# Performance work log

Measured on AMD Instinct MI355X. Metric: run time of the kernel, lower is better.

## Reference

```python
import jax, jax.numpy as jnp
import numpy as np

D_MODEL = 1024
N_HEADS = 16
D_HEAD = D_MODEL // N_HEADS
B, T = 4, 2048


def setup_inputs() -> dict:
    key = jax.random.key(0)
    ks = jax.random.split(key, 9)
    s = 0.02
    return {
        "x": jax.random.normal(ks[0], (B, T, D_MODEL), dtype=jnp.float32),
        "Wq": jax.random.normal(ks[1], (D_MODEL, D_MODEL), dtype=jnp.float32) * s,
        "bq": jnp.zeros((D_MODEL,), dtype=jnp.float32),
        "Wk": jax.random.normal(ks[2], (D_MODEL, D_MODEL), dtype=jnp.float32) * s,
        "bk": jnp.zeros((D_MODEL,), dtype=jnp.float32),
        "Wv": jax.random.normal(ks[3], (D_MODEL, D_MODEL), dtype=jnp.float32) * s,
        "bv": jnp.zeros((D_MODEL,), dtype=jnp.float32),
        "Wo": jax.random.normal(ks[4], (D_MODEL, D_MODEL), dtype=jnp.float32) * s,
        "bo": jnp.zeros((D_MODEL,), dtype=jnp.float32),
    }


def reference(x, Wq, bq, Wk, bk, Wv, bv, Wo, bo):
    # Dropout in eval mode (identity), as standard for a correctness baseline.
    Bx, Tx, _ = x.shape
    # torch nn.Linear: y = x @ W.T + b
    Q = x @ Wq.T + bq
    K = x @ Wk.T + bk
    V = x @ Wv.T + bv
    # [B, T, H, Dh] -> [B, H, T, Dh]
    Q = Q.reshape(Bx, Tx, N_HEADS, D_HEAD).transpose(0, 2, 1, 3)
    K = K.reshape(Bx, Tx, N_HEADS, D_HEAD).transpose(0, 2, 1, 3)
    V = V.reshape(Bx, Tx, N_HEADS, D_HEAD).transpose(0, 2, 1, 3)
    scale = 1.0 / jnp.sqrt(jnp.float32(D_HEAD))
    scores = jnp.einsum("bhqd,bhkd->bhqk", Q, K) * scale  # [B,H,T,T]
    # additive causal mask: -1e6 above the diagonal (matches torch.triu trick)
    mask = jnp.triu(jnp.full((Tx, Tx), -1000000.0, dtype=scores.dtype), k=1)
    scores = scores + mask
    attn = jax.nn.softmax(scores, axis=-1)
    out = jnp.einsum("bhqk,bhkd->bhqd", attn, V)  # [B,H,T,Dh]
    out = out.transpose(0, 2, 1, 3).reshape(Bx, Tx, D_MODEL)
    out = out @ Wo.T + bo
    return out
```

## Files before the change

### kernel.cpp

```cpp
#include <hip/hip_runtime.h>
#include <stdint.h>

#define DM 1024
#define HEADS 16
#define DH 64
#define BQ 4
#define TT 2048
#define MTOT (BQ*TT)
#define NQT (TT/64)

typedef __attribute__((ext_vector_type(8))) __bf16 bf16x8;
typedef __attribute__((ext_vector_type(4))) float f32x4;
typedef __attribute__((ext_vector_type(4))) uint32_t u32x4;
typedef unsigned short u16;
typedef __attribute__((ext_vector_type(8))) unsigned short u16x8;

__device__ __forceinline__ u16 f2b(float f) {
  uint32_t u = __builtin_bit_cast(uint32_t, f);
  u = (u + 0x7fffu + ((u >> 16) & 1u)) >> 16;
  return (u16)u;
}

__device__ __forceinline__ uint32_t cvtpk(float lo, float hi) {
  uint32_t r;
  asm("v_cvt_pk_bf16_f32 %0, %1, %2" : "=v"(r) : "v"(lo), "v"(hi));
  return r;
}

__device__ __forceinline__ void gload_lds16(const u16* g, u16* l) {
  __builtin_amdgcn_global_load_lds(
      (const __attribute__((address_space(1))) void*)g,
      (__attribute__((address_space(3))) void*)l, 16, 0, 0);
}

#define NX (MTOT * DM / 4)
#define NW (DM * DM / 4)
__global__ __launch_bounds__(256) void cast_all(const float* __restrict__ x,
                                                const float* __restrict__ Wq,
                                                const float* __restrict__ Wk,
                                                const float* __restrict__ Wv,
                                                const float* __restrict__ Wo,
                                                u16* __restrict__ xb,
                                                u16* __restrict__ wqkvb,
                                                u16* __restrict__ wob) {
  int i = blockIdx.x * 256 + threadIdx.x;
  const float* src; u16* dst;
  if (i < NX)               { src = x;  dst = xb; }
  else if (i < NX + NW)     { src = Wq; dst = wqkvb;          i -= NX; }
  else if (i < NX + 2 * NW) { src = Wk; dst = wqkvb + 4 * NW; i -= NX + NW; }
  else if (i < NX + 3 * NW) { src = Wv; dst = wqkvb + 8 * NW; i -= NX + 2 * NW; }
  else                      { src = Wo; dst = wob;            i -= NX + 3 * NW; }
  float4 v = ((const float4*)src)[i];
  ushort4 o;
  o.x = f2b(v.x); o.y = f2b(v.y); o.z = f2b(v.z); o.w = f2b(v.w);
  ((ushort4*)dst)[i] = o;
}

#define BKq 32
#define NKq (DM / BKq)
#define SLOT_A (256 * BKq)
#define SLOT_E (2 * SLOT_A)

__global__ __launch_bounds__(512, 2) void gemm_qkv8(const u16* __restrict__ A,
                                                    const u16* __restrict__ W,
                                                    const float* __restrict__ bq,
                                                    const float* __restrict__ bk,
                                                    const float* __restrict__ bv,
                                                    u16* __restrict__ Qo,
                                                    u16* __restrict__ Ko,
                                                    u16* __restrict__ Vto,
                                                    float qs) {
  __shared__ u16 lds[4 * SLOT_E];
  const int tid = threadIdx.x, lane = tid & 63, wave = tid >> 6;
  const int fr = lane & 15, g = lane >> 4;
  const int wm = wave >> 2, wn = wave & 3;

  int bid = blockIdx.x;
  bid = (bid & 7) * 48 + (bid >> 3);
  const int bx = bid % 12, by = bid / 12;
  const int m0 = by * 256, n0 = bx * 256;

  const int srow = tid >> 2;
  const int schunk = (tid & 3) ^ ((tid >> 3) & 3);
  const u16* gA0 = A + (size_t)(m0 + srow) * DM + schunk * 8;
  const u16* gA1 = gA0 + (size_t)128 * DM;
  const u16* gB0 = W + (size_t)(n0 + srow) * DM + schunk * 8;
  const u16* gB1 = gB0 + (size_t)128 * DM;
  const int dA0 = wave * 512;
  const int dA1 = 4096 + wave * 512;
  const int dB0 = SLOT_A + wave * 512;
  const int dB1 = SLOT_A + 4096 + wave * 512;

#define STAGEQ(slot, kt) {                                   \
    u16* ls = &lds[(slot) * SLOT_E];                         \
    const int ke = (kt) * BKq;                               \
    gload_lds16(gA0 + ke, ls + dA0);                         \
    gload_lds16(gA1 + ke, ls + dA1);                         \
    gload_lds16(gB0 + ke, ls + dB0);                         \
    gload_lds16(gB1 + ke, ls + dB1); }

  const int rchunk = (g ^ ((fr >> 1) & 3)) * 8;
  const int offA = (wm * 128 + fr) * 32 + rchunk;
  const int offB = SLOT_A + (wn * 64 + fr) * 32 + rchunk;

  f32x4 acc[8][4];
#pragma unroll
  for (int mi = 0; mi < 8; ++mi)
#pragma unroll
    for (int ni = 0; ni < 4; ++ni) acc[mi][ni] = (f32x4){0.f, 0.f, 0.f, 0.f};

  bf16x8 afA[8], bfA[4], afB[8], bfB[4];

#define READQ(AFv, BFv, kt) {                                \
    const u16* sl = &lds[((kt) & 3) * SLOT_E];               \
    _Pragma("unroll")                                        \
    for (int mi = 0; mi < 8; ++mi)                           \
      AFv[mi] = *(const bf16x8*)&sl[offA + mi * 512];        \
    _Pragma("unroll")                                        \
    for (int ni = 0; ni < 4; ++ni)                           \
      BFv[ni] = *(const bf16x8*)&sl[offB + ni * 512]; }

#define MFMAQ(AFv, BFv) {                                    \
    __builtin_amdgcn_s_setprio(1);                           \
    _Pragma("unroll")                                        \
    for (int mi = 0; mi < 8; ++mi)                           \
      _Pragma("unroll")                                      \
      for (int ni = 0; ni < 4; ++ni)                         \
        acc[mi][ni] = __builtin_amdgcn_mfma_f32_16x16x32_bf16(AFv[mi], BFv[ni], acc[mi][ni], 0, 0, 0); \
    __builtin_amdgcn_s_setprio(0); }

#define WAIT4 asm volatile("s_waitcnt vmcnt(4)" ::: "memory"); \
              asm volatile("s_barrier" ::: "memory");
#define WAIT0 asm volatile("s_waitcnt vmcnt(0)" ::: "memory"); \
              asm volatile("s_barrier" ::: "memory");

  STAGEQ(0, 0)
  STAGEQ(1, 1)
  STAGEQ(2, 2)
  asm volatile("s_waitcnt vmcnt(8)" ::: "memory");
  asm volatile("s_barrier" ::: "memory");
  READQ(afA, bfA, 0)

  for (int kt = 0; kt < NKq - 4; kt += 2) {
    WAIT4
    READQ(afB, bfB, kt + 1)
    MFMAQ(afA, bfA)
    STAGEQ((kt + 3) & 3, kt + 3)
    WAIT4
    READQ(afA, bfA, kt + 2)
    MFMAQ(afB, bfB)
    STAGEQ((kt + 4) & 3, kt + 4)
  }
  WAIT4
  READQ(afB, bfB, NKq - 3)
  MFMAQ(afA, bfA)
  STAGEQ((NKq - 1) & 3, NKq - 1)
  WAIT4
  READQ(afA, bfA, NKq - 2)
  MFMAQ(afB, bfB)
  WAIT0
  READQ(afB, bfB, NKq - 1)
  MFMAQ(afA, bfA)
  MFMAQ(afB, bfB)

  const int g4 = g * 4;
  const int seg = n0 >> 10;
  const int nbase = (n0 & 1023) + wn * 64 + fr;
  if (seg == 0) {
#pragma unroll
    for (int ni = 0; ni < 4; ++ni) {
      const int cgl = nbase + ni * 16;
      const float bb = bq[cgl];
      const int hh = cgl >> 6, d = cgl & 63;
#pragma unroll
      for (int mi = 0; mi < 8; ++mi) {
        const int m = m0 + wm * 128 + mi * 16 + g4;
        const int bi = m >> 11, t = m & 2047;
        u16* dst = &Qo[(((size_t)bi * HEADS + hh) * TT + t) * DH + d];
#pragma unroll
        for (int j = 0; j < 4; ++j)
          dst[(size_t)j * DH] = f2b((acc[mi][ni][j] + bb) * qs);
      }
    }
  } else if (seg == 1) {
#pragma unroll
    for (int ni = 0; ni < 4; ++ni) {
      const int cgl = nbase + ni * 16;
      const float bb = bk[cgl];
      const int hh = cgl >> 6, d = cgl & 63;
#pragma unroll
      for (int mi = 0; mi < 8; ++mi) {
        const int m = m0 + wm * 128 + mi * 16 + g4;
        const int bi = m >> 11, t = m & 2047;
        u16* dst = &Ko[(((size_t)bi * HEADS + hh) * TT + t) * DH + d];
#pragma unroll
        for (int j = 0; j < 4; ++j)
          dst[(size_t)j * DH] = f2b(acc[mi][ni][j] + bb);
      }
    }
  } else {
#pragma unroll
    for (int ni = 0; ni < 4; ++ni) {
      const int cgl = nbase + ni * 16;
      const float bb = bv[cgl];
      const int hh = cgl >> 6, d = cgl & 63;
#pragma unroll
      for (int mi = 0; mi < 8; ++mi) {
        const int t0 = (m0 + wm * 128 + mi * 16 + g4) & 2047;
        const int bi = (m0 + wm * 128 + mi * 16 + g4) >> 11;
        const int w64 = t0 & 63;
        const int pos = (t0 & ~63) | (((w64 >> 5) & 1) << 5) | (((w64 >> 2) & 3) << 3) |
                        (((w64 >> 4) & 1) << 2);
        ushort4 o;
        o.x = f2b(acc[mi][ni][0] + bb);
        o.y = f2b(acc[mi][ni][1] + bb);
        o.z = f2b(acc[mi][ni][2] + bb);
        o.w = f2b(acc[mi][ni][3] + bb);
        *(ushort4*)&Vto[(((size_t)bi * HEADS + hh) * DH + d) * TT + pos] = o;
      }
    }
  }
#undef STAGEQ
#undef READQ
#undef MFMAQ
#undef WAIT4
#undef WAIT0
}

__global__ __launch_bounds__(256) void gemm_out(const u16* __restrict__ A,
                                                const u16* __restrict__ Bw,
                                                const float* __restrict__ bias,
                                                float* __restrict__ outp) {
  __shared__ u16 As[128 * 32];
  __shared__ u16 Bs[128 * 32];
  const int tid = threadIdx.x;
  const int lane = tid & 63, wave = tid >> 6;
  const int wr = wave >> 1, wc = wave & 1;
  const int m0 = blockIdx.y * 128, n0 = blockIdx.x * 128;

  f32x4 acc[4][4];
#pragma unroll
  for (int m = 0; m < 4; ++m)
#pragma unroll
    for (int n = 0; n < 4; ++n) acc[m][n] = (f32x4){0.f, 0.f, 0.f, 0.f};

  const int srow = wave * 32 + (lane >> 2);
  const int scol = (lane & 3) * 8;
  const u16* gA = A + (size_t)(m0 + srow) * DM + scol;
  const u16* gB = Bw + (size_t)(n0 + srow) * DM + scol;
  u16* lA = &As[wave * 32 * 32];
  u16* lB = &Bs[wave * 32 * 32];
  const int fr = lane & 15;
  const int k8 = (lane >> 4) * 8;

  for (int k0 = 0; k0 < DM; k0 += 32) {
    __syncthreads();
    gload_lds16(gA + k0, lA);
    gload_lds16(gA + k0 + 16 * DM, lA + 16 * 32);
    gload_lds16(gB + k0, lB);
    gload_lds16(gB + k0 + 16 * DM, lB + 16 * 32);
    __syncthreads();
    bf16x8 af[4], bfr[4];
#pragma unroll
    for (int m = 0; m < 4; ++m)
      af[m] = *(const bf16x8*)&As[(wr * 64 + m * 16 + fr) * 32 + k8];
#pragma unroll
    for (int n = 0; n < 4; ++n)
      bfr[n] = *(const bf16x8*)&Bs[(wc * 64 + n * 16 + fr) * 32 + k8];
#pragma unroll
    for (int m = 0; m < 4; ++m)
#pragma unroll
      for (int n = 0; n < 4; ++n)
        acc[m][n] = __builtin_amdgcn_mfma_f32_16x16x32_bf16(af[m], bfr[n], acc[m][n], 0, 0, 0);
  }

#pragma unroll
  for (int m = 0; m < 4; ++m) {
    const int rg = m0 + wr * 64 + m * 16 + (lane >> 4) * 4;
#pragma unroll
    for (int n = 0; n < 4; ++n) {
      const int cg = n0 + wc * 64 + n * 16 + fr;
      const float bb = bias[cg];
#pragma unroll
      for (int j = 0; j < 4; ++j)
        outp[(size_t)(rg + j) * DM + cg] = acc[m][n][j] + bb;
    }
  }
}

__global__ __launch_bounds__(256) void attn_fwd(const u16* __restrict__ Q,
                                                const u16* __restrict__ K,
                                                const u16* __restrict__ Vt,
                                                u16* __restrict__ O) {
  const int o_ = blockIdx.x;
  const int r_ = o_ & 7, q_ = o_ >> 3;
  const int gidx = r_ * 8 + (q_ >> 4);
  const int pj = q_ & 15;
  const int b = gidx >> 4, h = gidx & 15;
  const int tid = threadIdx.x, lane = tid & 63, wave = tid >> 6;
  __shared__ u16 Ks[64 * 64];
  __shared__ u16 Vs[64 * 64];

  const size_t bh = ((size_t)b * HEADS + h) * TT;
  const size_t vbse = ((size_t)b * HEADS + h) * DH;
  const int fr = lane & 15, g = lane >> 4;
  const int sr = tid >> 2;
  const int sc0 = tid & 3;

  const int sw1 = (sc0 ^ (sr & 7)) * 8;
  const int sw2 = ((sc0 + 4) ^ (sr & 7)) * 8;
  const int sgc = sc0 * 8;
  const int rk0 = (g ^ (fr & 7)) * 8;
  const int rk1 = ((4 + g) ^ (fr & 7)) * 8;

  for (int pass = 0; pass < 2; ++pass) {
    const int qt = pass ? pj : (NQT - 1 - pj);
    const int q0 = qt * 64;
    const int qrow = q0 + wave * 16 + fr;
    const int k8 = g * 8;
    const bf16x8 qf0 = *(const bf16x8*)&Q[(bh + qrow) * DH + k8];
    const bf16x8 qf1 = *(const bf16x8*)&Q[(bh + qrow) * DH + 32 + k8];

    float lsum = 0.f;
    f32x4 oacc[4];
#pragma unroll
    for (int c = 0; c < 4; ++c) oacc[c] = (f32x4){0.f, 0.f, 0.f, 0.f};

    for (int kvb = 0; kvb <= qt; ++kvb) {
      const int kv0 = kvb * 64;
      {
        const u16* kg = &K[(bh + kv0 + sr) * DH + sgc];
        u16x8 ka = *(const u16x8*)kg;
        u16x8 kc = *(const u16x8*)(kg + 32);
        const u16* vg = &Vt[(vbse + sr) * TT + kv0 + sgc];
        u16x8 va = *(const u16x8*)vg;
        u16x8 vc = *(const u16x8*)(vg + 32);
        *(u16x8*)&Ks[sr * 64 + sw1] = ka;
        *(u16x8*)&Ks[sr * 64 + sw2] = kc;
        *(u16x8*)&Vs[sr * 64 + sw1] = va;
        *(u16x8*)&Vs[sr * 64 + sw2] = vc;
      }
      __syncthreads();

      f32x4 s[4];
      __builtin_amdgcn_s_setprio(1);
#pragma unroll
      for (int c = 0; c < 4; ++c) {
        bf16x8 kb0 = *(const bf16x8*)&Ks[(c * 16 + fr) * 64 + rk0];
        bf16x8 kb1 = *(const bf16x8*)&Ks[(c * 16 + fr) * 64 + rk1];
        f32x4 t = (f32x4){0.f, 0.f, 0.f, 0.f};
        t = __builtin_amdgcn_mfma_f32_16x16x32_bf16(kb0, qf0, t, 0, 0, 0);
        t = __builtin_amdgcn_mfma_f32_16x16x32_bf16(kb1, qf1, t, 0, 0, 0);
        s[c] = t;
      }
      __builtin_amdgcn_s_setprio(0);

      if (kvb == qt) {
#pragma unroll
        for (int c = 0; c < 4; ++c) {
          const int colg = kv0 + c * 16 + 4 * g;
#pragma unroll
          for (int r = 0; r < 4; ++r)
            if (colg + r > qrow) s[c][r] = -1e30f;
        }
      }

      float rs = 0.f;
      uint32_t pk[8];
#pragma unroll
      for (int c = 0; c < 4; ++c) {
        float p0 = __builtin_amdgcn_exp2f(s[c][0]);
        float p1 = __builtin_amdgcn_exp2f(s[c][1]);
        float p2 = __builtin_amdgcn_exp2f(s[c][2]);
        float p3 = __builtin_amdgcn_exp2f(s[c][3]);
        rs += (p0 + p1) + (p2 + p3);
        pk[2 * c] = cvtpk(p0, p1);
        pk[2 * c + 1] = cvtpk(p2, p3);
      }
      rs += __shfl_xor(rs, 16);
      rs += __shfl_xor(rs, 32);
      lsum += rs;

      const bf16x8 pa0 = __builtin_bit_cast(bf16x8, (u32x4){pk[0], pk[1], pk[2], pk[3]});
      const bf16x8 pa1 = __builtin_bit_cast(bf16x8, (u32x4){pk[4], pk[5], pk[6], pk[7]});

      __builtin_amdgcn_s_setprio(1);
#pragma unroll
      for (int c = 0; c < 4; ++c) {
        bf16x8 vb0 = *(const bf16x8*)&Vs[(c * 16 + fr) * 64 + rk0];
        bf16x8 vb1 = *(const bf16x8*)&Vs[(c * 16 + fr) * 64 + rk1];
        oacc[c] = __builtin_amdgcn_mfma_f32_16x16x32_bf16(vb0, pa0, oacc[c], 0, 0, 0);
        oacc[c] = __builtin_amdgcn_mfma_f32_16x16x32_bf16(vb1, pa1, oacc[c], 0, 0, 0);
      }
      __builtin_amdgcn_s_setprio(0);
      __syncthreads();
    }

    const float inv = 1.f / lsum;
#pragma unroll
    for (int c = 0; c < 4; ++c) {
      ushort4 o;
      o.x = f2b(oacc[c][0] * inv);
      o.y = f2b(oacc[c][1] * inv);
      o.z = f2b(oacc[c][2] * inv);
      o.w = f2b(oacc[c][3] * inv);
      *(ushort4*)&O[((size_t)b * TT + qrow) * DM + h * DH + c * 16 + 4 * g] = o;
    }
  }
}

extern "C" void kernel_launch(void* const* d_in, const int* in_sizes, int n_in,
                              void* d_out, int out_size, void* d_ws, size_t ws_size,
                              hipStream_t stream) {
  const float* x  = (const float*)d_in[0];
  const float* Wq = (const float*)d_in[1];
  const float* bq = (const float*)d_in[2];
  const float* Wk = (const float*)d_in[3];
  const float* bk = (const float*)d_in[4];
  const float* Wv = (const float*)d_in[5];
  const float* bv = (const float*)d_in[6];
  const float* Wo = (const float*)d_in[7];
  const float* bo = (const float*)d_in[8];

  char* w = (char*)d_ws;
  u16* xb    = (u16*)w; w += (size_t)MTOT * DM * 2;
  u16* Wqkvb = (u16*)w; w += (size_t)3 * DM * DM * 2;
  u16* Wob   = (u16*)w; w += (size_t)DM * DM * 2;
  u16* Qb    = (u16*)w; w += (size_t)MTOT * DM * 2;
  u16* Kb    = (u16*)w; w += (size_t)MTOT * DM * 2;
  u16* Vtb   = (u16*)w; w += (size_t)MTOT * DM * 2;
  u16* AOb   = (u16*)w; w += (size_t)MTOT * DM * 2;

  cast_all<<<(NX + 4 * NW) / 256, 256, 0, stream>>>(x, Wq, Wk, Wv, Wo, xb, Wqkvb, Wob);

  const float qs = 0.125f * 1.44269504f;
  gemm_qkv8<<<384, 512, 0, stream>>>(xb, Wqkvb, bq, bk, bv, Qb, Kb, Vtb, qs);

  attn_fwd<<<1024, 256, 0, stream>>>(Qb, Kb, Vtb, AOb);

  gemm_out<<<dim3(DM / 128, MTOT / 128), 256, 0, stream>>>(AOb, Wob, bo, (float*)d_out);
}
```

Measured before the change: 166.3 us.

## Pipeline output projection GEMM with multi-stage LDS and split QKV stage loop

Replaces the simple single-buffered output-projection GEMM with a 512-thread, 256x128-tile kernel that uses a 4-slot direct-to-LDS prefetch pipeline with swizzled reads and counted vmcnt waits. It also splits each QKV GEMM k-step into two halves, with an extra barrier so the A and B tile loads are issued between MFMA halves. The aim is to hide global-load latency and remove per-step full syncs. The trade-offs are more LDS per block, which may limit occupancy, and extra barriers in the QKV loop.

```diff
diff --git a/kernel.cpp b/kernel.cpp
--- a/kernel.cpp
+++ b/kernel.cpp
@@ -91,11 +91,14 @@
   const int dB0 = SLOT_A + wave * 512;
   const int dB1 = SLOT_A + 4096 + wave * 512;
 
-#define STAGEQ(slot, kt) {                                   \
+#define STAGE_Ah(slot, kt) {                                 \
     u16* ls = &lds[(slot) * SLOT_E];                         \
     const int ke = (kt) * BKq;                               \
     gload_lds16(gA0 + ke, ls + dA0);                         \
-    gload_lds16(gA1 + ke, ls + dA1);                         \
+    gload_lds16(gA1 + ke, ls + dA1); }
+#define STAGE_Bh(slot, kt) {                                 \
+    u16* ls = &lds[(slot) * SLOT_E];                         \
+    const int ke = (kt) * BKq;                               \
     gload_lds16(gB0 + ke, ls + dB0);                         \
     gload_lds16(gB1 + ke, ls + dB1); }
 
@@ -111,57 +114,73 @@
 
   bf16x8 afA[8], bfA[4], afB[8], bfB[4];
 
-#define READQ(AFv, BFv, kt) {                                \
+#define READ_P1(AFv, BFv, kt) {                              \
     const u16* sl = &lds[((kt) & 3) * SLOT_E];               \
     _Pragma("unroll")                                        \
-    for (int mi = 0; mi < 8; ++mi)                           \
+    for (int mi = 0; mi < 4; ++mi)                           \
       AFv[mi] = *(const bf16x8*)&sl[offA + mi * 512];        \
     _Pragma("unroll")                                        \
     for (int ni = 0; ni < 4; ++ni)                           \
       BFv[ni] = *(const bf16x8*)&sl[offB + ni * 512]; }
-
-#define MFMAQ(AFv, BFv) {                                    \
+#define READ_P2(AFv, kt) {                                   \
+    const u16* sl = &lds[((kt) & 3) * SLOT_E];               \
+    _Pragma("unroll")                                        \
+    for (int mi = 4; mi < 8; ++mi)                           \
+      AFv[mi] = *(const bf16x8*)&sl[offA + mi * 512]; }
+
+#define MFMA_P1(AFv, BFv) {                                  \
     __builtin_amdgcn_s_setprio(1);                           \
     _Pragma("unroll")                                        \
-    for (int mi = 0; mi < 8; ++mi)                           \
+    for (int mi = 0; mi < 4; ++mi)                           \
       _Pragma("unroll")                                      \
       for (int ni = 0; ni < 4; ++ni)                         \
         acc[mi][ni] = __builtin_amdgcn_mfma_f32_16x16x32_bf16(AFv[mi], BFv[ni], acc[mi][ni], 0, 0, 0); \
     __builtin_amdgcn_s_setprio(0); }
-
-#define WAIT4 asm volatile("s_waitcnt vmcnt(4)" ::: "memory"); \
-              asm volatile("s_barrier" ::: "memory");
-#define WAIT0 asm volatile("s_waitcnt vmcnt(0)" ::: "memory"); \
-              asm volatile("s_barrier" ::: "memory");
-
-  STAGEQ(0, 0)
-  STAGEQ(1, 1)
-  STAGEQ(2, 2)
+#define MFMA_P2(AFv, BFv) {                                  \
+    __builtin_amdgcn_s_setprio(1);                           \
+    _Pragma("unroll")                                        \
+    for (int mi = 4; mi < 8; ++mi)                           \
+      _Pragma("unroll")                                      \
+      for (int ni = 0; ni < 4; ++ni)                         \
+        acc[mi][ni] = __builtin_amdgcn_mfma_f32_16x16x32_bf16(AFv[mi], BFv[ni], acc[mi][ni], 0, 0, 0); \
+    __builtin_amdgcn_s_setprio(0); }
+
+#define BARQ asm volatile("s_barrier" ::: "memory");
+#define WAIT4 asm volatile("s_waitcnt vmcnt(4)" ::: "memory"); BARQ
+#define WAIT0 asm volatile("s_waitcnt vmcnt(0)" ::: "memory"); BARQ
+
+#define STEP(AFc, BFc, AFn, BFn, kt, DO_STAGE) {             \
+    WAIT4                                                    \
+    READ_P1(AFn, BFn, (kt) + 1)                              \
+    MFMA_P1(AFc, BFc)                                        \
+    if (DO_STAGE) STAGE_Ah(((kt) + 3) & 3, (kt) + 3)         \
+    BARQ                                                     \
+    READ_P2(AFn, (kt) + 1)                                   \
+    MFMA_P2(AFc, BFc)                                        \
+    if (DO_STAGE) STAGE_Bh(((kt) + 3) & 3, (kt) + 3) }
+
+  STAGE_Ah(0, 0) STAGE_Bh(0, 0)
+  STAGE_Ah(1, 1) STAGE_Bh(1, 1)
+  STAGE_Ah(2, 2) STAGE_Bh(2, 2)
   asm volatile("s_waitcnt vmcnt(8)" ::: "memory");
   asm volatile("s_barrier" ::: "memory");
-  READQ(afA, bfA, 0)
+  READ_P1(afA, bfA, 0)
+  READ_P2(afA, 0)
 
   for (int kt = 0; kt < NKq - 4; kt += 2) {
-    WAIT4
-    READQ(afB, bfB, kt + 1)
-    MFMAQ(afA, bfA)
-    STAGEQ((kt + 3) & 3, kt + 3)
-    WAIT4
-    READQ(afA, bfA, kt + 2)
-    MFMAQ(afB, bfB)
-    STAGEQ((kt + 4) & 3, kt + 4)
+    STEP(afA, bfA, afB, bfB, kt, true)
+    STEP(afB, bfB, afA, bfA, kt + 1, true)
   }
-  WAIT4
-  READQ(afB, bfB, NKq - 3)
-  MFMAQ(afA, bfA)
-  STAGEQ((NKq - 1) & 3, NKq - 1)
-  WAIT4
-  READQ(afA, bfA, NKq - 2)
-  MFMAQ(afB, bfB)
+  STEP(afA, bfA, afB, bfB, NKq - 4, true)
+  STEP(afB, bfB, afA, bfA, NKq - 3, false)
   WAIT0
-  READQ(afB, bfB, NKq - 1)
-  MFMAQ(afA, bfA)
-  MFMAQ(afB, bfB)
+  READ_P1(afB, bfB, NKq - 1)
+  MFMA_P1(afA, bfA)
+  BARQ
+  READ_P2(afB, NKq - 1)
+  MFMA_P2(afA, bfA)
+  MFMA_P1(afB, bfB)
+  MFMA_P2(afB, bfB)
 
   const int g4 = g * 4;
   const int seg = n0 >> 10;
@@ -220,72 +239,132 @@
       }
     }
   }
-#undef STAGEQ
-#undef READQ
-#undef MFMAQ
+#undef STAGE_Ah
+#undef STAGE_Bh
+#undef READ_P1
+#undef READ_P2
+#undef MFMA_P1
+#undef MFMA_P2
+#undef STEP
+#undef BARQ
 #undef WAIT4
 #undef WAIT0
 }
 
-__global__ __launch_bounds__(256) void gemm_out(const u16* __restrict__ A,
-                                                const u16* __restrict__ Bw,
-                                                const float* __restrict__ bias,
-                                                float* __restrict__ outp) {
-  __shared__ u16 As[128 * 32];
-  __shared__ u16 Bs[128 * 32];
-  const int tid = threadIdx.x;
-  const int lane = tid & 63, wave = tid >> 6;
-  const int wr = wave >> 1, wc = wave & 1;
-  const int m0 = blockIdx.y * 128, n0 = blockIdx.x * 128;
+#define SLOT_OA (256 * 32)
+#define SLOT_OB (128 * 32)
+#define SLOT_OE (SLOT_OA + SLOT_OB)
+
+__global__ __launch_bounds__(512, 2) void gemm_out8(const u16* __restrict__ A,
+                                                    const u16* __restrict__ Bw,
+                                                    const float* __restrict__ bias,
+                                                    float* __restrict__ outp) {
+  __shared__ u16 lds[4 * SLOT_OE];
+  const int tid = threadIdx.x, lane = tid & 63, wave = tid >> 6;
+  const int fr = lane & 15, g = lane >> 4;
+  const int wm = wave >> 1, wn = wave & 1;
+
+  const int bx = blockIdx.x >> 5, by = blockIdx.x & 31;
+  const int m0 = by * 256, n0 = bx * 128;
+
+  const int srow = tid >> 2;
+  const int schunk = (tid & 3) ^ ((tid >> 3) & 3);
+  const u16* gA0 = A + (size_t)(m0 + srow) * DM + schunk * 8;
+  const u16* gA1 = gA0 + (size_t)128 * DM;
+  const u16* gB0 = Bw + (size_t)(n0 + srow) * DM + schunk * 8;
+  const int dA0 = wave * 512;
+  const int dA1 = 4096 + wave * 512;
+  const int dB0 = SLOT_OA + wave * 512;
+
+#define STAGEO(slot, kt) {                                   \
+    u16* ls = &lds[(slot) * SLOT_OE];                        \
+    const int ke = (kt) * 32;                                \
+    gload_lds16(gA0 + ke, ls + dA0);                         \
+    gload_lds16(gA1 + ke, ls + dA1);                         \
+    gload_lds16(gB0 + ke, ls + dB0); }
+
+  const int rchunk = (g ^ ((fr >> 1) & 3)) * 8;
+  const int offA = (wm * 64 + fr) * 32 + rchunk;
+  const int offB = SLOT_OA + (wn * 64 + fr) * 32 + rchunk;
 
   f32x4 acc[4][4];
 #pragma unroll
-  for (int m = 0; m < 4; ++m)
-#pragma unroll
-    for (int n = 0; n < 4; ++n) acc[m][n] = (f32x4){0.f, 0.f, 0.f, 0.f};
-
-  const int srow = wave * 32 + (lane >> 2);
-  const int scol = (lane & 3) * 8;
-  const u16* gA = A + (size_t)(m0 + srow) * DM + scol;
-  const u16* gB = Bw + (size_t)(n0 + srow) * DM + scol;
-  u16* lA = &As[wave * 32 * 32];
-  u16* lB = &Bs[wave * 32 * 32];
-  const int fr = lane & 15;
-  const int k8 = (lane >> 4) * 8;
-
-  for (int k0 = 0; k0 < DM; k0 += 32) {
-    __syncthreads();
-    gload_lds16(gA + k0, lA);
-    gload_lds16(gA + k0 + 16 * DM, lA + 16 * 32);
-    gload_lds16(gB + k0, lB);
-    gload_lds16(gB + k0 + 16 * DM, lB + 16 * 32);
-    __syncthreads();
-    bf16x8 af[4], bfr[4];
-#pragma unroll
-    for (int m = 0; m < 4; ++m)
-      af[m] = *(const bf16x8*)&As[(wr * 64 + m * 16 + fr) * 32 + k8];
-#pragma unroll
-    for (int n = 0; n < 4; ++n)
-      bfr[n] = *(const bf16x8*)&Bs[(wc * 64 + n * 16 + fr) * 32 + k8];
-#pragma unroll
-    for (int m = 0; m < 4; ++m)
-#pragma unroll
-      for (int n = 0; n < 4; ++n)
-        acc[m][n] = __builtin_amdgcn_mfma_f32_16x16x32_bf16(af[m], bfr[n], acc[m][n], 0, 0, 0);
+  for (int mi = 0; mi < 4; ++mi)
+#pragma unroll
+    for (int ni = 0; ni < 4; ++ni) acc[mi][ni] = (f32x4){0.f, 0.f, 0.f, 0.f};
+
+  bf16x8 afA[4], bfA[4], afB[4], bfB[4];
+
+#define READO(AFv, BFv, kt) {                                \
+    const u16* sl = &lds[((kt) & 3) * SLOT_OE];              \
+    _Pragma("unroll")                                        \
+    for (int mi = 0; mi < 4; ++mi)                           \
+      AFv[mi] = *(const bf16x8*)&sl[offA + mi * 512];        \
+    _Pragma("unroll")                                        \
+    for (int ni = 0; ni < 4; ++ni)                           \
+      BFv[ni] = *(const bf16x8*)&sl[offB + ni * 512]; }
+
+#define MFMAO(AFv, BFv) {                                    \
+    __builtin_amdgcn_s_setprio(1);                           \
+    _Pragma("unroll")                                        \
+    for (int mi = 0; mi < 4; ++mi)                           \
+      _Pragma("unroll")                                      \
+      for (int ni = 0; ni < 4; ++ni)                         \
+        acc[mi][ni] = __builtin_amdgcn_mfma_f32_16x16x32_bf16(AFv[mi], BFv[ni], acc[mi][ni], 0, 0, 0); \
+    __builtin_amdgcn_s_setprio(0); }
+
+#define OW3 asm volatile("s_waitcnt vmcnt(3)" ::: "memory"); \
+            asm volatile("s_barrier" ::: "memory");
+#define OW0 asm volatile("s_waitcnt vmcnt(0)" ::: "memory"); \
+            asm volatile("s_barrier" ::: "memory");
+
+  STAGEO(0, 0)
+  STAGEO(1, 1)
+  STAGEO(2, 2)
+  asm volatile("s_waitcnt vmcnt(6)" ::: "memory");
+  asm volatile("s_barrier" ::: "memory");
+  READO(afA, bfA, 0)
+
+  for (int kt = 0; kt < 28; kt += 2) {
+    OW3
+    READO(afB, bfB, kt + 1)
+    MFMAO(afA, bfA)
+    STAGEO((kt + 3) & 3, kt + 3)
+    OW3
+    READO(afA, bfA, kt + 2)
+    MFMAO(afB, bfB)
+    STAGEO((kt + 4) & 3, kt + 4)
   }
-
-#pragma unroll
-  for (int m = 0; m < 4; ++m) {
-    const int rg = m0 + wr * 64 + m * 16 + (lane >> 4) * 4;
-#pragma unroll
-    for (int n = 0; n < 4; ++n) {
-      const int cg = n0 + wc * 64 + n * 16 + fr;
+  OW3
+  READO(afB, bfB, 29)
+  MFMAO(afA, bfA)
+  STAGEO(3, 31)
+  OW3
+  READO(afA, bfA, 30)
+  MFMAO(afB, bfB)
+  OW0
+  READO(afB, bfB, 31)
+  MFMAO(afA, bfA)
+  MFMAO(afB, bfB)
+
+  const int g4 = g * 4;
+#pragma unroll
+  for (int mi = 0; mi < 4; ++mi) {
+    const int rg = m0 + wm * 64 + mi * 16 + g4;
+#pragma unroll
+    for (int ni = 0; ni < 4; ++ni) {
+      const int cg = n0 + wn * 64 + ni * 16 + fr;
       const float bb = bias[cg];
 #pragma unroll
       for (int j = 0; j < 4; ++j)
-        outp[(size_t)(rg + j) * DM + cg] = acc[m][n][j] + bb;
+        outp[(size_t)(rg + j) * DM + cg] = acc[mi][ni][j] + bb;
     }
   }
+#undef STAGEO
+#undef READO
+#undef MFMAO
+#undef OW3
+#undef OW0
 }
 
 __global__ __launch_bounds__(256) void attn_fwd(const u16* __restrict__ Q,
@@ -438,5 +517,5 @@
 
   attn_fwd<<<1024, 256, 0, stream>>>(Qb, Kb, Vtb, AOb);
 
-  gemm_out<<<dim3(DM / 128, MTOT / 128), 256, 0, stream>>>(AOb, Wob, bo, (float*)d_out);
-}
+  gemm_out8<<<256, 512, 0, stream>>>(AOb, Wob, bo, (float*)d_out);
+}
```

New measurement: 161.0 us. 1.03x faster.
